# Kernel optimization log

Hardware: AMD Instinct MI355X
Metric: run time of the kernel (lower is better)

The kernel has to match this reference:

```python
import jax, jax.numpy as jnp
import numpy as np

NUM_DOCS = 1024  # fill_max of doc_indices

def setup_inputs() -> dict:
    key = jax.random.key(0)
    k1, k2, k3 = jax.random.split(key, 3)
    N, D, E = 262144, 1024, 64
    x = jax.random.normal(k1, (N, D), dtype=jnp.float32)
    doc_indices = jax.random.randint(k2, (N,), 0, NUM_DOCS, dtype=jnp.int64)
    W_gate = jax.random.normal(k3, (E, D), dtype=jnp.float32)
    return {"x": x, "doc_indices": doc_indices, "W_gate": W_gate}

def reference(x, doc_indices, W_gate):
    # gate linear + softmax: [N, E]
    logits = jnp.einsum('nd,ed->ne', x, W_gate)
    w = jax.nn.softmax(logits, axis=-1)

    seg = doc_indices.astype(jnp.int32)
    E = w.shape[-1]
    # one-pass segment reductions replacing the per-document Python loop
    sum_w = jax.ops.segment_sum(w, seg, num_segments=NUM_DOCS)          # [D, E]
    sum_w2 = jax.ops.segment_sum(w * w, seg, num_segments=NUM_DOCS)     # [D, E]
    counts = jax.ops.segment_sum(jnp.ones_like(w[:, :1]), seg, num_segments=NUM_DOCS)  # [D, 1]
    safe_n = jnp.maximum(counts, 1.0)
    centroid = sum_w / safe_n                                            # [D, E]
    # per-doc sum of squared deviations: sum(w^2) - n * centroid^2
    ssd = jnp.sum(sum_w2 - safe_n * centroid * centroid, axis=-1)        # [D]
    n = counts[:, 0]
    per_doc_mse = ssd / (safe_n[:, 0] * E)                               # mean over n_d*E elements
    valid = n > 1.0                                                      # docs with >1 token contribute
    penalty_sum = jnp.sum(jnp.where(valid, per_doc_mse, 0.0))
    num_unique = jnp.sum((n > 0.0).astype(jnp.float32))
    doc_penalty = penalty_sum / num_unique
    return (w, doc_penalty)
```

## Files before the change

### kernel.cpp

```cpp
#include <hip/hip_runtime.h>
#include <math.h>

#define NROWS 262144
#define DDIM  1024
#define EEXP  64
#define NDOCS 1024
#define BM    128
#define HB    64
#define RPB   (NROWS / HB)
#define NGEMM (NROWS / BM)

typedef __attribute__((ext_vector_type(8)))  __bf16 bf16x8;
typedef __attribute__((ext_vector_type(16))) float  f32x16;
typedef unsigned short ushort_t;
typedef unsigned int   uint_t;


__global__ __launch_bounds__(256) void conv_hist_kernel(const float* __restrict__ Wg,
                                                        ushort_t* __restrict__ Wf,
                                                        const int* __restrict__ idx,
                                                        int* __restrict__ hist_slices) {
    if (blockIdx.x < 512) {
        const int i = blockIdx.x * 256 + threadIdx.x;
        const int j = i & 7;
        const int l = (i >> 3) & 63;
        const int f = (i >> 9) & 7;
        const int T = i >> 12;
        const int cl = l & 31;
        const int hi = l >> 5;
        const int e  = cl + 32 * ((f >> 1) & 1);
        const int k  = T * 32 + 16 * (f & 1) + 8 * hi + j;
        const float wv = Wg[e * DDIM + k];
        const uint_t b = __float_as_uint(wv);
        ushort_t out;
        if (f < 4) {
            out = (ushort_t)(b >> 16);
        } else {
            const float lov = wv - __uint_as_float(b & 0xFFFF0000u);
            out = (ushort_t)(__float_as_uint(lov) >> 16);
        }
        Wf[i] = out;
    } else {
        __shared__ int lh[NDOCS];
        const int bh = blockIdx.x - 512;
        const int t  = threadIdx.x;
        for (int i = t; i < NDOCS; i += 256) lh[i] = 0;
        __syncthreads();
        const int base = bh * RPB;
        for (int i = t; i < RPB; i += 256) atomicAdd(&lh[idx[base + i]], 1);
        __syncthreads();
        for (int i = t; i < NDOCS; i += 256) hist_slices[bh * NDOCS + i] = lh[i];
    }
}

__global__ __launch_bounds__(1024) void scan_kernel(const int* __restrict__ hist_slices,
                                                    int* __restrict__ offsets,
                                                    int* __restrict__ cursor,
                                                    float* __restrict__ pen_sum,
                                                    float* __restrict__ uniq,
                                                    int* __restrict__ done_count) {
    __shared__ int sbuf[NDOCS];
    const int t = threadIdx.x;
    int my = 0;
    #pragma unroll 4
    for (int b = 0; b < HB; ++b) my += hist_slices[b * NDOCS + t];
    sbuf[t] = my;
    __syncthreads();
    for (int off = 1; off < NDOCS; off <<= 1) {
        int add = (t >= off) ? sbuf[t - off] : 0;
        __syncthreads();
        sbuf[t] += add;
        __syncthreads();
    }
    const int excl = sbuf[t] - my;
    offsets[t] = excl;
    cursor[t]  = excl;
    if (t == NDOCS - 1) offsets[NDOCS] = sbuf[t];
    if (t == 0) { pen_sum[0] = 0.0f; uniq[0] = 0.0f; done_count[0] = 0; }
}

__device__ __forceinline__ void gl2lds16(const float* g, float* l) {
    __builtin_amdgcn_global_load_lds(
        (const __attribute__((address_space(1))) void*)g,
        (__attribute__((address_space(3))) void*)l,
        16, 0, 0);
}

#define VMCNT(N)  asm volatile("s_waitcnt vmcnt(" #N ")" ::: "memory")

struct WT { bf16x8 h00, h01, h10, h11, m00, m01, m10, m11; };

__global__ __launch_bounds__(256, 2) void gemm_scatter_kernel(
    const float*    __restrict__ x,
    const ushort_t* __restrict__ Wf,
    const int*      __restrict__ idx,
    int*            __restrict__ cursor,
    int*            __restrict__ sorted_rows,
    float*          __restrict__ w_out)
{
    __shared__ float xs[2][8192];

    if (blockIdx.x >= NGEMM) {
        int* lh    = (int*)&xs[0][0];
        int* lbase = lh + NDOCS;
        int* lc    = lbase + NDOCS;
        const int bh = blockIdx.x - NGEMM;
        const int t  = threadIdx.x;
        for (int i = t; i < NDOCS; i += 256) { lh[i] = 0; lc[i] = 0; }
        __syncthreads();
        const int base = bh * RPB;
        for (int i = t; i < RPB; i += 256) atomicAdd(&lh[idx[base + i]], 1);
        __syncthreads();
        for (int i = t; i < NDOCS; i += 256) {
            const int c = lh[i];
            if (c) lbase[i] = atomicAdd(&cursor[i], c);
        }
        __syncthreads();
        for (int i = t; i < RPB; i += 256) {
            const int r = base + i;
            const int d = idx[r];
            const int p = atomicAdd(&lc[d], 1);
            sorted_rows[lbase[d] + p] = r;
        }
        return;
    }

    const int t   = threadIdx.x;
    const int w   = t >> 6;
    const int l   = t & 63;
    const int cl  = l & 31;
    const int hi  = l >> 5;
    const size_t br = (size_t)blockIdx.x * BM;

    f32x16 acc0 = {};
    f32x16 acc1 = {};
    WT wA, wB;

    union u8b { uint_t u[4]; bf16x8 v; };

#define LOAD_WF(DST, T2) do {                                                          \
        const ushort_t* p_ = Wf + ((size_t)(T2) * 8 * 64 + l) * 8;                     \
        DST.h00 = *(const bf16x8*)(p_ + 0 * 512);                                      \
        DST.h01 = *(const bf16x8*)(p_ + 1 * 512);                                      \
        DST.h10 = *(const bf16x8*)(p_ + 2 * 512);                                      \
        DST.h11 = *(const bf16x8*)(p_ + 3 * 512);                                      \
        DST.m00 = *(const bf16x8*)(p_ + 4 * 512);                                      \
        DST.m01 = *(const bf16x8*)(p_ + 5 * 512);                                      \
        DST.m10 = *(const bf16x8*)(p_ + 6 * 512);                                      \
        DST.m11 = *(const bf16x8*)(p_ + 7 * 512);                                      \
    } while (0)

#define STAGE_X2(BUF, SUP) do {                                                        \
        float* xb_ = &xs[BUF][w * 2048];                                               \
        _Pragma("unroll")                                                              \
        for (int i_ = 0; i_ < 8; ++i_) {                                               \
            const int row_ = i_ * 4 + (l >> 4);                                        \
            const int u_   = (l & 15) ^ (row_ & 15);                                   \
            const float* gp_ = x + (br + w * 32 + row_) * DDIM + (SUP) * 64 + u_ * 4;  \
            gl2lds16(gp_, xb_ + i_ * 256);                                             \
        } } while (0)

#define SPLIT8(A, B, AH, AL) do {                                                      \
        const float av_[8] = {A.x, A.y, A.z, A.w, B.x, B.y, B.z, B.w};                 \
        _Pragma("unroll")                                                              \
        for (int p_ = 0; p_ < 4; ++p_) {                                               \
            const uint_t b0_ = __float_as_uint(av_[2 * p_]);                           \
            const uint_t b1_ = __float_as_uint(av_[2 * p_ + 1]);                       \
            AH.u[p_] = (b0_ >> 16) | (b1_ & 0xFFFF0000u);                              \
            const float l0_ = av_[2 * p_]     - __uint_as_float(b0_ & 0xFFFF0000u);    \
            const float l1_ = av_[2 * p_ + 1] - __uint_as_float(b1_ & 0xFFFF0000u);    \
            AL.u[p_] = (__float_as_uint(l0_) >> 16) | (__float_as_uint(l1_) & 0xFFFF0000u); \
        } } while (0)

#define COMPUTE(BUF, TT, WV) do {                                                      \
        const float* xb_ = &xs[BUF][w * 2048];                                         \
        const int blk_ = (cl >> 2) * 256 + (cl & 3) * 64;                              \
        const int ku_  = (TT) * 8 + hi * 2;                                            \
        const int sw_  = cl & 15;                                                      \
        const float4 a0_ = *(const float4*)&xb_[blk_ + (((ku_ + 0) ^ sw_) * 4)];       \
        const float4 a1_ = *(const float4*)&xb_[blk_ + (((ku_ + 1) ^ sw_) * 4)];       \
        const float4 a2_ = *(const float4*)&xb_[blk_ + (((ku_ + 4) ^ sw_) * 4)];       \
        const float4 a3_ = *(const float4*)&xb_[blk_ + (((ku_ + 5) ^ sw_) * 4)];       \
        u8b ah0, al0, ah1, al1;                                                        \
        SPLIT8(a0_, a1_, ah0, al0);                                                    \
        SPLIT8(a2_, a3_, ah1, al1);                                                    \
        acc0 = __builtin_amdgcn_mfma_f32_32x32x16_bf16(ah0.v, WV.h00, acc0, 0, 0, 0);  \
        acc1 = __builtin_amdgcn_mfma_f32_32x32x16_bf16(ah0.v, WV.h10, acc1, 0, 0, 0);  \
        acc0 = __builtin_amdgcn_mfma_f32_32x32x16_bf16(ah0.v, WV.m00, acc0, 0, 0, 0);  \
        acc1 = __builtin_amdgcn_mfma_f32_32x32x16_bf16(ah0.v, WV.m10, acc1, 0, 0, 0);  \
        acc0 = __builtin_amdgcn_mfma_f32_32x32x16_bf16(al0.v, WV.h00, acc0, 0, 0, 0);  \
        acc1 = __builtin_amdgcn_mfma_f32_32x32x16_bf16(al0.v, WV.h10, acc1, 0, 0, 0);  \
        acc0 = __builtin_amdgcn_mfma_f32_32x32x16_bf16(ah1.v, WV.h01, acc0, 0, 0, 0);  \
        acc1 = __builtin_amdgcn_mfma_f32_32x32x16_bf16(ah1.v, WV.h11, acc1, 0, 0, 0);  \
        acc0 = __builtin_amdgcn_mfma_f32_32x32x16_bf16(ah1.v, WV.m01, acc0, 0, 0, 0);  \
        acc1 = __builtin_amdgcn_mfma_f32_32x32x16_bf16(ah1.v, WV.m11, acc1, 0, 0, 0);  \
        acc0 = __builtin_amdgcn_mfma_f32_32x32x16_bf16(al1.v, WV.h01, acc0, 0, 0, 0);  \
        acc1 = __builtin_amdgcn_mfma_f32_32x32x16_bf16(al1.v, WV.h11, acc1, 0, 0, 0);  \
    } while (0)

    const int s0  = ((int)blockIdx.x * 5 + w) & 15;
    const int sP1 = (s0 + 1) & 15;

    LOAD_WF(wA, 2 * s0);
    STAGE_X2(0, s0);
    LOAD_WF(wB, 2 * s0 + 1);
    STAGE_X2(1, sP1);
    VMCNT(16);
    COMPUTE(0, 0, wA);
    LOAD_WF(wA, 2 * sP1);
    VMCNT(16);
    COMPUTE(0, 1, wB);

    #pragma unroll 1
    for (int S = 1; S < 15; ++S) {
        const int cb   = S & 1;
        const int scur = (s0 + S) & 15;
        const int snxt = (s0 + S + 1) & 15;
        LOAD_WF(wB, 2 * scur + 1);
        STAGE_X2(cb ^ 1, snxt);
        VMCNT(16);
        COMPUTE(cb, 0, wA);
        LOAD_WF(wA, 2 * snxt);
        VMCNT(16);
        COMPUTE(cb, 1, wB);
    }
    {
        const int slast = (s0 + 15) & 15;
        LOAD_WF(wB, 2 * slast + 1);
        VMCNT(8);
        COMPUTE(1, 0, wA);
        VMCNT(0);
        COMPUTE(1, 1, wB);
    }

    const size_t orow_base = br + (size_t)w * 32;
    #pragma unroll
    for (int r = 0; r < 16; ++r) {
        const int row = (r & 3) + 8 * (r >> 2) + 4 * hi;
        const float v0 = acc0[r];
        const float v1 = acc1[r];
        float m = fmaxf(v0, v1);
        m = fmaxf(m, __shfl_xor(m, 1));
        m = fmaxf(m, __shfl_xor(m, 2));
        m = fmaxf(m, __shfl_xor(m, 4));
        m = fmaxf(m, __shfl_xor(m, 8));
        m = fmaxf(m, __shfl_xor(m, 16));
        const float e0 = __expf(v0 - m);
        const float e1 = __expf(v1 - m);
        float s = e0 + e1;
        s += __shfl_xor(s, 1);
        s += __shfl_xor(s, 2);
        s += __shfl_xor(s, 4);
        s += __shfl_xor(s, 8);
        s += __shfl_xor(s, 16);
        const float inv = 1.0f / s;
        float* wo = w_out + (orow_base + row) * EEXP;
        wo[cl]      = e0 * inv;
        wo[32 + cl] = e1 * inv;
    }
#undef LOAD_WF
#undef STAGE_X2
#undef SPLIT8
#undef COMPUTE
}

__global__ __launch_bounds__(256) void segsum_final_kernel(
    const float* __restrict__ w,
    const int*   __restrict__ sorted_rows,
    const int*   __restrict__ offsets,
    float*       __restrict__ pen_sum,
    float*       __restrict__ uniq,
    int*         __restrict__ done_count,
    float*       __restrict__ pen_out)
{
    __shared__ int rows_s[512];
    __shared__ float ls1[4][64], ls2[4][64];

    const int d  = blockIdx.x;
    const int t  = threadIdx.x;
    const int e  = t & 63;
    const int rg = t >> 6;
    const int start = offsets[d];
    const int end   = offsets[d + 1];
    const int n     = end - start;

    for (int i = t; i < n && i < 512; i += 256) rows_s[i] = sorted_rows[start + i];
    __syncthreads();

    float s1 = 0.0f, s2 = 0.0f;
    for (int i = rg; i < n; i += 4) {
        const int row = (i < 512) ? rows_s[i] : sorted_rows[start + i];
        const float v = w[(size_t)row * EEXP + e];
        s1 += v;
        s2 += v * v;
    }

    ls1[rg][e] = s1;
    ls2[rg][e] = s2;
    __syncthreads();

    if (t < 64) {
        const float a = ls1[0][e] + ls1[1][e] + ls1[2][e] + ls1[3][e];
        const float b = ls2[0][e] + ls2[1][e] + ls2[2][e] + ls2[3][e];
        const float safe = fmaxf((float)n, 1.0f);
        float contrib = b - a * a / safe;
        #pragma unroll
        for (int off = 32; off > 0; off >>= 1)
            contrib += __shfl_down(contrib, off);
        if (e == 0) {
            if (n > 1) atomicAdd(pen_sum, contrib / (safe * (float)EEXP));
            if (n > 0) atomicAdd(uniq, 1.0f);
        }
    }
    __syncthreads();
    if (t == 0) {
        __threadfence();
        const int prev = atomicAdd(done_count, 1);
        if (prev == NDOCS - 1) {
            __threadfence();
            pen_out[0] = pen_sum[0] / uniq[0];
        }
    }
}

extern "C" void kernel_launch(void* const* d_in, const int* in_sizes, int n_in,
                              void* d_out, int out_size, void* d_ws, size_t ws_size,
                              hipStream_t stream) {
    const float* x   = (const float*)d_in[0];
    const int*   idx = (const int*)d_in[1];
    const float* Wg  = (const float*)d_in[2];

    float* out   = (float*)d_out;
    float* w_out = out;
    float* pen   = out + (size_t)NROWS * EEXP;

    ushort_t* Wf     = (ushort_t*)d_ws;
    int* hist_slices = (int*)(Wf + 131072);
    int* sorted_rows = hist_slices + HB * NDOCS;
    int* offsets     = sorted_rows + NROWS;
    int* cursor      = offsets + NDOCS + 1;
    float* pen_sum   = (float*)(cursor + NDOCS);
    float* uniq      = pen_sum + 1;
    int* done_count  = (int*)(uniq + 1);

    conv_hist_kernel<<<512 + HB, 256, 0, stream>>>(Wg, Wf, idx, hist_slices);
    scan_kernel<<<1, 1024, 0, stream>>>(hist_slices, offsets, cursor, pen_sum, uniq, done_count);
    gemm_scatter_kernel<<<NGEMM + HB, 256, 0, stream>>>(x, Wf, idx, cursor, sorted_rows, w_out);
    segsum_final_kernel<<<NDOCS, 256, 0, stream>>>(w_out, sorted_rows, offsets, pen_sum, uniq, done_count, pen);
}
```

Baseline: 338.6 us.

## Double K-chunk per stage to 128 and quad-buffer gate weight registers

Each pipeline stage now stages 128 columns of x per row instead of 64, doubling the LDS buffer to 128 KB, and keeps four register sets of gate weights so four MFMA sub-steps run per stage. This halves the number of stages and gives each wait more in-flight loads, aiming to hide global latency better. The cost is occupancy: launch bounds drop to one block per CU, LDS use doubles and register pressure rises, and the VMCNT thresholds had to be retuned by hand, which risks ordering mistakes.

Result: slower. 374.6 us (+10.6%).

```diff
diff --git a/kernel.cpp b/kernel.cpp
--- a/kernel.cpp
+++ b/kernel.cpp
@@ -90,7 +90,7 @@
 
 struct WT { bf16x8 h00, h01, h10, h11, m00, m01, m10, m11; };
 
-__global__ __launch_bounds__(256, 2) void gemm_scatter_kernel(
+__global__ __launch_bounds__(256, 1) void gemm_scatter_kernel(
     const float*    __restrict__ x,
     const ushort_t* __restrict__ Wf,
     const int*      __restrict__ idx,
@@ -98,7 +98,7 @@
     int*            __restrict__ sorted_rows,
     float*          __restrict__ w_out)
 {
-    __shared__ float xs[2][8192];
+    __shared__ float xs[2][16384];
 
     if (blockIdx.x >= NGEMM) {
         int* lh    = (int*)&xs[0][0];
@@ -134,7 +134,7 @@
 
     f32x16 acc0 = {};
     f32x16 acc1 = {};
-    WT wA, wB;
+    WT w0, w1, w2, w3;
 
     union u8b { uint_t u[4]; bf16x8 v; };
 
@@ -151,12 +151,12 @@
     } while (0)
 
 #define STAGE_X2(BUF, SUP) do {                                                        \
-        float* xb_ = &xs[BUF][w * 2048];                                               \
+        float* xb_ = &xs[BUF][w * 4096];                                               \
         _Pragma("unroll")                                                              \
-        for (int i_ = 0; i_ < 8; ++i_) {                                               \
-            const int row_ = i_ * 4 + (l >> 4);                                        \
-            const int u_   = (l & 15) ^ (row_ & 15);                                   \
-            const float* gp_ = x + (br + w * 32 + row_) * DDIM + (SUP) * 64 + u_ * 4;  \
+        for (int i_ = 0; i_ < 16; ++i_) {                                              \
+            const int row_ = i_ * 2 + (l >> 5);                                        \
+            const int u_   = (l & 31) ^ (row_ & 15);                                   \
+            const float* gp_ = x + (br + w * 32 + row_) * DDIM + (SUP) * 128 + u_ * 4; \
             gl2lds16(gp_, xb_ + i_ * 256);                                             \
         } } while (0)
 
@@ -173,8 +173,8 @@
         } } while (0)
 
 #define COMPUTE(BUF, TT, WV) do {                                                      \
-        const float* xb_ = &xs[BUF][w * 2048];                                         \
-        const int blk_ = (cl >> 2) * 256 + (cl & 3) * 64;                              \
+        const float* xb_ = &xs[BUF][w * 4096];                                         \
+        const int blk_ = (cl >> 1) * 256 + (cl & 1) * 128;                             \
         const int ku_  = (TT) * 8 + hi * 2;                                            \
         const int sw_  = cl & 15;                                                      \
         const float4 a0_ = *(const float4*)&xb_[blk_ + (((ku_ + 0) ^ sw_) * 4)];       \
@@ -198,39 +198,43 @@
         acc1 = __builtin_amdgcn_mfma_f32_32x32x16_bf16(al1.v, WV.h11, acc1, 0, 0, 0);  \
     } while (0)
 
-    const int s0  = ((int)blockIdx.x * 5 + w) & 15;
-    const int sP1 = (s0 + 1) & 15;
-
-    LOAD_WF(wA, 2 * s0);
+    const int s0 = ((int)blockIdx.x * 5 + w) & 7;
+
     STAGE_X2(0, s0);
-    LOAD_WF(wB, 2 * s0 + 1);
-    STAGE_X2(1, sP1);
-    VMCNT(16);
-    COMPUTE(0, 0, wA);
-    LOAD_WF(wA, 2 * sP1);
-    VMCNT(16);
-    COMPUTE(0, 1, wB);
+    LOAD_WF(w0, 4 * s0);
 
     #pragma unroll 1
-    for (int S = 1; S < 15; ++S) {
+    for (int S = 0; S < 7; ++S) {
         const int cb   = S & 1;
-        const int scur = (s0 + S) & 15;
-        const int snxt = (s0 + S + 1) & 15;
-        LOAD_WF(wB, 2 * scur + 1);
+        const int scur = (s0 + S) & 7;
+        const int snxt = (s0 + S + 1) & 7;
+        LOAD_WF(w1, 4 * scur + 1);
+        LOAD_WF(w2, 4 * scur + 2);
+        LOAD_WF(w3, 4 * scur + 3);
+        VMCNT(24);
+        COMPUTE(cb, 0, w0);
         STAGE_X2(cb ^ 1, snxt);
+        VMCNT(32);
+        COMPUTE(cb, 1, w1);
+        VMCNT(24);
+        COMPUTE(cb, 2, w2);
+        LOAD_WF(w0, 4 * snxt);
+        VMCNT(24);
+        COMPUTE(cb, 3, w3);
+    }
+    {
+        const int slast = (s0 + 7) & 7;
+        LOAD_WF(w1, 4 * slast + 1);
+        LOAD_WF(w2, 4 * slast + 2);
+        LOAD_WF(w3, 4 * slast + 3);
+        VMCNT(24);
+        COMPUTE(1, 0, w0);
         VMCNT(16);
-        COMPUTE(cb, 0, wA);
-        LOAD_WF(wA, 2 * snxt);
-        VMCNT(16);
-        COMPUTE(cb, 1, wB);
-    }
-    {
-        const int slast = (s0 + 15) & 15;
-        LOAD_WF(wB, 2 * slast + 1);
+        COMPUTE(1, 1, w1);
         VMCNT(8);
-        COMPUTE(1, 0, wA);
+        COMPUTE(1, 2, w2);
         VMCNT(0);
-        COMPUTE(1, 1, wB);
+        COMPUTE(1, 3, w3);
     }
 
     const size_t orow_base = br + (size_t)w * 32;
```
